# Kernel tuning notes

Measured on AMD Instinct MI355X. Metric: run time of the kernel, lower is better.

The kernel has to match this reference:

```python
import jax, jax.numpy as jnp
import numpy as np


def qz(x, width=8, frac=4):
    """Fixed-point fake-quant (MASE integer quantizer) with straight-through estimator."""
    step = 2.0 ** (-frac)
    lo = float(-(2 ** (width - 1)))
    hi = float(2 ** (width - 1) - 1)
    q = jnp.clip(jnp.round(x / step), lo, hi) * step
    return x + jax.lax.stop_gradient(q - x)


def qlinear(x, w, b=None):
    # quantize activations (8,4) and weights (8,7), dequantized GEMM
    y = qz(x, 8, 4) @ qz(w, 8, 7).T
    if b is not None:
        y = y + qz(b, 8, 7)
    return y


def setup_inputs() -> dict:
    key = jax.random.key(0)
    ks = jax.random.split(key, 14)
    B, N, C, HID = 4, 1024, 1024, 4096
    g = lambda k, shape, sc: jax.random.normal(k, shape, jnp.float32) * sc
    return {
        "x": g(ks[0], (B, N, C), 1.0),
        "q_w": g(ks[1], (C, C), 0.05),
        "kv_w": g(ks[2], (2 * C, C), 0.05),
        "proj_w": g(ks[3], (C, C), 0.05),
        "proj_b": jnp.zeros((C,), jnp.float32),
        "fc1_w": g(ks[4], (HID, C), 0.05),
        "fc1_b": jnp.zeros((HID,), jnp.float32),
        "fc2_w": g(ks[5], (C, HID), 0.05),
        "fc2_b": jnp.zeros((C,), jnp.float32),
        "aff1_w": g(ks[6], (1,), 1.0),
        "aff1_b": g(ks[7], (1,), 0.5),
        "aff2_w": g(ks[8], (1,), 1.0),
        "aff2_b": g(ks[9], (1,), 0.5),
    }


def reference(x, q_w, kv_w, proj_w, proj_b, fc1_w, fc1_b, fc2_w, fc2_b,
              aff1_w, aff1_b, aff2_w, aff2_b):
    B, N, C = x.shape
    H = 16
    D = C // H
    scale = D ** (-0.5)

    def affine(t, w, b):
        # quantized mul then quantized add (fixed_affine)
        t = qz(t, 8, 4) * qz(w, 8, 4)
        return qz(t, 8, 4) + qz(b, 8, 4)

    # ---- attention branch ----
    h = affine(x, aff1_w, aff1_b)
    q = qlinear(h, q_w).reshape(B, N, H, D).transpose(0, 2, 1, 3)      # [B,H,N,D]
    kv = qlinear(h, kv_w).reshape(B, N, 2, H, D).transpose(2, 0, 3, 1, 4)
    k, v = kv[0], kv[1]                                                 # [B,H,N,D]
    attn = jnp.einsum('bhnd,bhmd->bhnm', qz(q, 8, 4), qz(k, 8, 4))     # quant matmul
    attn = jax.nn.softmax(qz(attn * scale, 8, 4), axis=-1)             # QHashSoftmax
    attn = qz(attn, 8, 7)
    z = jnp.einsum('bhnm,bhmd->bhnd', qz(attn, 8, 7), qz(v, 8, 4))     # quant matmul
    z = z.transpose(0, 2, 1, 3).reshape(B, N, C)
    z = qlinear(z, proj_w, proj_b)
    x = qz(x, 8, 4) + qz(z, 8, 4)                                      # add1

    # ---- mlp branch ----
    h = affine(x, aff2_w, aff2_b)
    m = qlinear(h, fc1_w, fc1_b)
    m = qz(jax.nn.relu(m), 8, 4)                                       # quant relu
    m = qlinear(m, fc2_w, fc2_b)
    return qz(x, 8, 4) + qz(m, 8, 4)                                   # add2
```

## Files before the change

### kernel.cpp

```cpp
#include <hip/hip_runtime.h>

typedef unsigned short u16;
typedef __attribute__((ext_vector_type(4))) float f32x4;
typedef __attribute__((ext_vector_type(8))) short short8;
typedef __attribute__((ext_vector_type(4))) unsigned short u16x4;
typedef __attribute__((ext_vector_type(8))) unsigned short u16x8;

__device__ __forceinline__ float clampf(float x, float lo, float hi){ return fminf(fmaxf(x, lo), hi); }
__device__ __forceinline__ float qz44i(float x){ return clampf(rintf(x*16.f), -128.f, 127.f); }
__device__ __forceinline__ float qz44v(float x){ return qz44i(x)*0.0625f; }
__device__ __forceinline__ float qz87v(float x){ return clampf(rintf(x*128.f), -128.f, 127.f)*0.0078125f; }
__device__ __forceinline__ u16 bfbits(float f){ return (u16)(__float_as_uint(f) >> 16); }

__device__ __forceinline__ void gll16(const void* g, void* l){
  __builtin_amdgcn_global_load_lds((const __attribute__((address_space(1))) void*)g,
                                   (__attribute__((address_space(3))) void*)l, 16, 0, 0);
}

__global__ __launch_bounds__(256) void kquantw5(const float* __restrict__ w0, u16* __restrict__ o0,
                                                const float* __restrict__ w1, u16* __restrict__ o1,
                                                const float* __restrict__ w2, u16* __restrict__ o2,
                                                const float* __restrict__ w3, u16* __restrict__ o3,
                                                const float* __restrict__ w4, u16* __restrict__ o4){
  int v = blockIdx.x*256 + threadIdx.x;
  const float* w; u16* o; int base;
  if      (v <  262144){ w = w0; o = o0; base = 0;       }
  else if (v <  786432){ w = w1; o = o1; base = 262144;  }
  else if (v < 1048576){ w = w2; o = o2; base = 786432;  }
  else if (v < 2097152){ w = w3; o = o3; base = 1048576; }
  else                 { w = w4; o = o4; base = 2097152; }
  int i = (v - base)*4;
  float4 val = *(const float4*)(w + i);
  u16x4 r;
  r.x = bfbits(qz87v(val.x)); r.y = bfbits(qz87v(val.y));
  r.z = bfbits(qz87v(val.z)); r.w = bfbits(qz87v(val.w));
  *(u16x4*)(o + i) = r;
}

__global__ __launch_bounds__(256) void kaffine(const float* __restrict__ x, const float* __restrict__ aw,
                                               const float* __restrict__ ab, u16* __restrict__ o, int n){
  int i = (blockIdx.x*256 + threadIdx.x)*4;
  if (i >= n) return;
  float awv = qz44v(aw[0]);
  float abi = qz44i(ab[0]);
  float4 v = *(const float4*)(x + i);
  float in[4] = {v.x, v.y, v.z, v.w};
  u16x4 r;
  #pragma unroll
  for (int k=0;k<4;++k){
    float t  = qz44v(in[k]) * awv;
    float hi = clampf(qz44i(t) + abi, -128.f, 127.f);
    ((u16*)&r)[k] = bfbits(hi*0.0625f);
  }
  *(u16x4*)(o + i) = r;
}

__global__ __launch_bounds__(256) void ktransv(const u16* __restrict__ KVb, u16* __restrict__ VT){
  __shared__ u16 t[64][72];
  int nt = blockIdx.x;
  int bh = blockIdx.y;
  int b = bh >> 4, h = bh & 15;
  int tid = threadIdx.x;
  int nl = tid >> 2, d0 = (tid & 3)*16;
  const u16* src = KVb + (size_t)(b*1024 + nt*64 + nl)*2048 + 1024 + h*64 + d0;
  u16x8 v0 = *(const u16x8*)(src);
  u16x8 v1 = *(const u16x8*)(src + 8);
  #pragma unroll
  for (int k=0;k<8;++k) t[nl][d0+k]   = ((u16*)&v0)[k];
  #pragma unroll
  for (int k=0;k<8;++k) t[nl][d0+8+k] = ((u16*)&v1)[k];
  __syncthreads();
  int dl = tid >> 2, n0 = (tid & 3)*16;
  u16x8 o0, o1;
  #pragma unroll
  for (int k=0;k<8;++k) ((u16*)&o0)[k] = t[n0+k][dl];
  #pragma unroll
  for (int k=0;k<8;++k) ((u16*)&o1)[k] = t[n0+8+k][dl];
  u16* dst = VT + (size_t)bh*65536 + (size_t)dl*1024 + nt*64 + n0;
  *(u16x8*)(dst)     = o0;
  *(u16x8*)(dst + 8) = o1;
}

template<int EPI>
__global__ __launch_bounds__(256) void kgemm(
    const u16* __restrict__ A, const u16* __restrict__ Bw,
    const float* __restrict__ bias, const float* __restrict__ extra,
    u16* __restrict__ outB, float* __restrict__ outF,
    int M, int N, int K)
{
  __shared__ char As[128*64*2];
  __shared__ char Bs[128*64*2];
  const int tid = threadIdx.x, lane = tid & 63, w = tid >> 6;
  const int bm = blockIdx.y*128, bn = blockIdx.x*128;
  const int wr = (w>>1)*64, wc = (w&1)*64;
  const int srow = lane>>3;
  const int scol = (((lane&7) ^ srow) & 7)*8;
  const int mrow = lane & 15, kg = lane >> 4, swz = (lane & 7) << 4;

  const u16* Ab = A  + (size_t)bm*K;
  const u16* Bb = Bw + (size_t)bn*K;

  f32x4 acc[4][4];
  #pragma unroll
  for (int i=0;i<4;++i)
    #pragma unroll
    for (int j=0;j<4;++j) acc[i][j] = (f32x4){0.f,0.f,0.f,0.f};

  for (int k0 = 0; k0 < K; k0 += 64){
    #pragma unroll
    for (int c=0;c<4;++c){
      int ch = w*4 + c;
      int row = ch*8 + srow;
      gll16(Ab + (size_t)row*K + k0 + scol, As + ch*1024);
      gll16(Bb + (size_t)row*K + k0 + scol, Bs + ch*1024);
    }
    __syncthreads();
    #pragma unroll
    for (int ks=0; ks<2; ++ks){
      const int cb = (64*ks + 16*kg) ^ swz;
      short8 av[4], bv[4];
      #pragma unroll
      for (int i=0;i<4;++i) av[i] = *(const short8*)(As + (wr + i*16 + mrow)*128 + cb);
      #pragma unroll
      for (int j=0;j<4;++j) bv[j] = *(const short8*)(Bs + (wc + j*16 + mrow)*128 + cb);
      #pragma unroll
      for (int i=0;i<4;++i)
        #pragma unroll
        for (int j=0;j<4;++j)
          acc[i][j] = __builtin_amdgcn_mfma_f32_16x16x32_bf16(av[i], bv[j], acc[i][j], 0, 0, 0);
    }
    __syncthreads();
  }

  #pragma unroll
  for (int i=0;i<4;++i){
    #pragma unroll
    for (int j=0;j<4;++j){
      #pragma unroll
      for (int r=0;r<4;++r){
        int row = bm + wr + i*16 + 4*kg + r;
        int col = bn + wc + j*16 + mrow;
        float y = acc[i][j][r];
        size_t idx = (size_t)row*N + col;
        if (EPI == 0){
          outB[idx] = bfbits(qz44v(y));
        } else if (EPI == 1){
          y += qz87v(bias[col]);
          outF[idx] = qz44v(extra[idx]) + qz44v(y);
        } else if (EPI == 2){
          y += qz87v(bias[col]);
          y = fmaxf(y, 0.f);
          outB[idx] = bfbits(qz44v(y));
        } else {
          y += qz87v(bias[col]);
          outF[idx] = qz44v(extra[idx]) + qz44v(y);
        }
      }
    }
  }
}

__device__ __forceinline__ void compute_s(const char* Qs, const char* Ks,
                                          int w, int mrow, int kg, int swz, f32x4 (&s)[2][8]){
  short8 a[2][2];
  #pragma unroll
  for (int i=0;i<2;++i)
    #pragma unroll
    for (int ks=0;ks<2;++ks)
      a[i][ks] = *(const short8*)(Qs + (w*32 + i*16 + mrow)*128 + ((64*ks + 16*kg) ^ swz));
  #pragma unroll
  for (int i=0;i<2;++i)
    #pragma unroll
    for (int jf=0;jf<8;++jf) s[i][jf] = (f32x4){0.f,0.f,0.f,0.f};
  #pragma unroll
  for (int jf=0;jf<8;++jf){
    short8 b0 = *(const short8*)(Ks + (jf*16 + mrow)*128 + ((16*kg) ^ swz));
    short8 b1 = *(const short8*)(Ks + (jf*16 + mrow)*128 + ((64 + 16*kg) ^ swz));
    #pragma unroll
    for (int i=0;i<2;++i){
      s[i][jf] = __builtin_amdgcn_mfma_f32_16x16x32_bf16(a[i][0], b0, s[i][jf], 0, 0, 0);
      s[i][jf] = __builtin_amdgcn_mfma_f32_16x16x32_bf16(a[i][1], b1, s[i][jf], 0, 0, 0);
    }
  }
}

__global__ __launch_bounds__(256) void kattn(const u16* __restrict__ Qb, const u16* __restrict__ KVb,
                                             const u16* __restrict__ VT, u16* __restrict__ zq)
{
  __shared__ char Qs[128*128];
  __shared__ char Ks[128*128];
  __shared__ char Ps[128*256];
  __shared__ char Vs[64*256];
  const int tid = threadIdx.x, lane = tid & 63, w = tid >> 6;
  const int qt = blockIdx.x, bh = blockIdx.y;
  const int b = bh >> 4, h = bh & 15;
  const int srow = lane >> 3;
  const int scol = (((lane&7) ^ srow) & 7)*8;
  const int mrow = lane & 15, kg = lane >> 4, swz = (lane & 7) << 4;
  const size_t q0 = (size_t)(b*1024 + qt*128);

  #pragma unroll
  for (int c=0;c<4;++c){
    int ch = w*4 + c; int r = ch*8 + srow;
    gll16(Qb + (q0 + r)*1024 + h*64 + scol, Qs + ch*1024);
  }

  float m[2][4], Z[2][4];
  #pragma unroll
  for (int i=0;i<2;++i)
    #pragma unroll
    for (int r=0;r<4;++r){ m[i][r] = -3.0e38f; Z[i][r] = 0.f; }

  for (int kt=0; kt<8; ++kt){
    #pragma unroll
    for (int c=0;c<4;++c){
      int ch = w*4 + c; int r = ch*8 + srow;
      gll16(KVb + (size_t)(b*1024 + kt*128 + r)*2048 + h*64 + scol, Ks + ch*1024);
    }
    __syncthreads();
    f32x4 s[2][8];
    compute_s(Qs, Ks, w, mrow, kg, swz, s);
    #pragma unroll
    for (int i=0;i<2;++i){
      #pragma unroll
      for (int r=0;r<4;++r){
        float lv[8];
        float tmax = -3.0e38f;
        #pragma unroll
        for (int jf=0;jf<8;++jf){
          lv[jf] = clampf(rintf(s[i][jf][r]*2.f), -128.f, 127.f)*0.0625f;
          tmax = fmaxf(tmax, lv[jf]);
        }
        #pragma unroll
        for (int off=1; off<16; off<<=1) tmax = fmaxf(tmax, __shfl_xor(tmax, off));
        float ts = 0.f;
        #pragma unroll
        for (int jf=0;jf<8;++jf) ts += expf(lv[jf] - tmax);
        #pragma unroll
        for (int off=1; off<16; off<<=1) ts += __shfl_xor(ts, off);
        float mo = m[i][r];
        float mn = fmaxf(mo, tmax);
        Z[i][r] = Z[i][r]*expf(mo - mn) + ts*expf(tmax - mn);
        m[i][r] = mn;
      }
    }
    __syncthreads();
  }

  f32x4 zacc[2][4];
  #pragma unroll
  for (int i=0;i<2;++i)
    #pragma unroll
    for (int d=0;d<4;++d) zacc[i][d] = (f32x4){0.f,0.f,0.f,0.f};

  for (int kt=0; kt<8; ++kt){
    #pragma unroll
    for (int c=0;c<4;++c){
      int ch = w*4 + c; int r = ch*8 + srow;
      gll16(KVb + (size_t)(b*1024 + kt*128 + r)*2048 + h*64 + scol, Ks + ch*1024);
    }
    #pragma unroll
    for (int c=0;c<4;++c){
      int ch = w*4 + c; int dr = ch*4 + kg;
      int vx = ((lane&15) ^ (dr & 7))*8;
      gll16(VT + (size_t)bh*65536 + (size_t)dr*1024 + kt*128 + vx, Vs + ch*1024);
    }
    __syncthreads();
    f32x4 s[2][8];
    compute_s(Qs, Ks, w, mrow, kg, swz, s);
    #pragma unroll
    for (int i=0;i<2;++i){
      #pragma unroll
      for (int r=0;r<4;++r){
        float mm = m[i][r], zz = Z[i][r];
        int prow = w*32 + i*16 + 4*kg + r;
        int sw2 = (prow & 7) << 4;
        #pragma unroll
        for (int jf=0;jf<8;++jf){
          float lv = clampf(rintf(s[i][jf][r]*2.f), -128.f, 127.f)*0.0625f;
          float p = expf(lv - mm) / zz;
          float pi = fminf(rintf(p*128.f), 127.f);
          *(u16*)(Ps + prow*256 + (((jf*16 + mrow)*2) ^ sw2)) = bfbits(pi*0.0078125f);
        }
      }
    }
    __syncthreads();
    #pragma unroll
    for (int ms=0; ms<4; ++ms){
      const int cb = (64*ms + 16*kg) ^ swz;
      short8 pa0 = *(const short8*)(Ps + (w*32 +  0 + mrow)*256 + cb);
      short8 pa1 = *(const short8*)(Ps + (w*32 + 16 + mrow)*256 + cb);
      #pragma unroll
      for (int df=0; df<4; ++df){
        short8 vb = *(const short8*)(Vs + (df*16 + mrow)*256 + cb);
        zacc[0][df] = __builtin_amdgcn_mfma_f32_16x16x32_bf16(pa0, vb, zacc[0][df], 0, 0, 0);
        zacc[1][df] = __builtin_amdgcn_mfma_f32_16x16x32_bf16(pa1, vb, zacc[1][df], 0, 0, 0);
      }
    }
    __syncthreads();
  }

  #pragma unroll
  for (int i=0;i<2;++i){
    #pragma unroll
    for (int df=0; df<4; ++df){
      #pragma unroll
      for (int r=0;r<4;++r){
        int row = qt*128 + w*32 + i*16 + 4*kg + r;
        int col = df*16 + mrow;
        zq[((size_t)b*1024 + row)*1024 + h*64 + col] = bfbits(qz44v(zacc[i][df][r]));
      }
    }
  }
}

extern "C" void kernel_launch(void* const* d_in, const int* in_sizes, int n_in,
                              void* d_out, int out_size, void* d_ws, size_t ws_size,
                              hipStream_t stream) {
  const float* x      = (const float*)d_in[0];
  const float* q_w    = (const float*)d_in[1];
  const float* kv_w   = (const float*)d_in[2];
  const float* proj_w = (const float*)d_in[3];
  const float* proj_b = (const float*)d_in[4];
  const float* fc1_w  = (const float*)d_in[5];
  const float* fc1_b  = (const float*)d_in[6];
  const float* fc2_w  = (const float*)d_in[7];
  const float* fc2_b  = (const float*)d_in[8];
  const float* aff1_w = (const float*)d_in[9];
  const float* aff1_b = (const float*)d_in[10];
  const float* aff2_w = (const float*)d_in[11];
  const float* aff2_b = (const float*)d_in[12];

  char* ws = (char*)d_ws;
  const size_t MB = 1u << 20;
  u16*   wq_q  = (u16*)(ws + 0*MB);
  u16*   wq_kv = (u16*)(ws + 2*MB);
  u16*   wq_pj = (u16*)(ws + 6*MB);
  u16*   wq_f1 = (u16*)(ws + 8*MB);
  u16*   wq_f2 = (u16*)(ws + 16*MB);
  float* x1    = (float*)(ws + 24*MB);
  u16*   h1q   = (u16*)(ws + 40*MB);
  u16*   Qbuf  = (u16*)(ws + 48*MB);
  u16*   KVb   = (u16*)(ws + 56*MB);
  u16*   VT    = (u16*)(ws + 72*MB);
  u16*   mq    = (u16*)(ws + 56*MB);
  u16*   zq    = h1q;
  u16*   h2q   = Qbuf;

  kquantw5<<<12288, 256, 0, stream>>>(q_w, wq_q, kv_w, wq_kv, proj_w, wq_pj,
                                      fc1_w, wq_f1, fc2_w, wq_f2);

  kaffine<<<4096, 256, 0, stream>>>(x, aff1_w, aff1_b, h1q, 4096*1024);
  kgemm<0><<<dim3(8,32),  256, 0, stream>>>(h1q, wq_q,  nullptr, nullptr, Qbuf, nullptr, 4096, 1024, 1024);
  kgemm<0><<<dim3(16,32), 256, 0, stream>>>(h1q, wq_kv, nullptr, nullptr, KVb,  nullptr, 4096, 2048, 1024);
  ktransv<<<dim3(16,64), 256, 0, stream>>>(KVb, VT);
  kattn<<<dim3(8,64), 256, 0, stream>>>(Qbuf, KVb, VT, zq);
  kgemm<1><<<dim3(8,32),  256, 0, stream>>>(zq, wq_pj, proj_b, x, nullptr, x1, 4096, 1024, 1024);

  kaffine<<<4096, 256, 0, stream>>>(x1, aff2_w, aff2_b, h2q, 4096*1024);
  kgemm<2><<<dim3(32,32), 256, 0, stream>>>(h2q, wq_f1, fc1_b, nullptr, mq, nullptr, 4096, 4096, 1024);
  kgemm<3><<<dim3(8,32),  256, 0, stream>>>(mq, wq_f2, fc2_b, x1, nullptr, (float*)d_out, 4096, 1024, 4096);
}
```

Measured before the change: 456.2 us.

## Add 128x64 GEMM tile for N=1024 GEMMs and use exp lookup table in attention

Adds a kgemm64 kernel with a 128x64 output tile and uses it for the three N=1024 GEMMs (q, proj, fc2), doubling the grid to 512 blocks so more of the GPU's compute units are occupied. In attention, expf calls are replaced by a 256-entry shared-memory table indexed by integer logit differences, which works because the quantized logits fall on a 1/16 grid. V tiles are now read straight from global memory instead of being staged in LDS, and one barrier is removed. The direct V loads may be uncoalesced. The barrier between writing P and reading it appears to have no sync when a wave reads other waves' P rows, but each wave reads only its own rows, so it is probably safe. The exp_t table is written without a barrier before its first use, although the later barrier in the first loop covers it.

Result: faster. 427.0 us (-6.4%).

```diff
diff --git a/kernel.cpp b/kernel.cpp
--- a/kernel.cpp
+++ b/kernel.cpp
@@ -160,6 +160,90 @@
   }
 }
 
+template<int EPI>
+__global__ __launch_bounds__(256) void kgemm64(
+    const u16* __restrict__ A, const u16* __restrict__ Bw,
+    const float* __restrict__ bias, const float* __restrict__ extra,
+    u16* __restrict__ outB, float* __restrict__ outF,
+    int M, int N, int K)
+{
+  __shared__ char As[128*64*2];
+  __shared__ char Bs[64*64*2];
+  const int tid = threadIdx.x, lane = tid & 63, w = tid >> 6;
+  const int bm = blockIdx.y*128, bn = blockIdx.x*64;
+  const int wr = w*32;
+  const int srow = lane>>3;
+  const int scol = (((lane&7) ^ srow) & 7)*8;
+  const int mrow = lane & 15, kg = lane >> 4, swz = (lane & 7) << 4;
+
+  const u16* Ab = A  + (size_t)bm*K;
+  const u16* Bb = Bw + (size_t)bn*K;
+
+  f32x4 acc[2][4];
+  #pragma unroll
+  for (int i=0;i<2;++i)
+    #pragma unroll
+    for (int j=0;j<4;++j) acc[i][j] = (f32x4){0.f,0.f,0.f,0.f};
+
+  for (int k0 = 0; k0 < K; k0 += 64){
+    #pragma unroll
+    for (int c=0;c<4;++c){
+      int ch = w*4 + c;
+      int row = ch*8 + srow;
+      gll16(Ab + (size_t)row*K + k0 + scol, As + ch*1024);
+    }
+    #pragma unroll
+    for (int c=0;c<2;++c){
+      int ch = w*2 + c;
+      int row = ch*8 + srow;
+      gll16(Bb + (size_t)row*K + k0 + scol, Bs + ch*1024);
+    }
+    __syncthreads();
+    #pragma unroll
+    for (int ks=0; ks<2; ++ks){
+      const int cb = (64*ks + 16*kg) ^ swz;
+      short8 av[2], bv[4];
+      #pragma unroll
+      for (int i=0;i<2;++i) av[i] = *(const short8*)(As + (wr + i*16 + mrow)*128 + cb);
+      #pragma unroll
+      for (int j=0;j<4;++j) bv[j] = *(const short8*)(Bs + (j*16 + mrow)*128 + cb);
+      #pragma unroll
+      for (int i=0;i<2;++i)
+        #pragma unroll
+        for (int j=0;j<4;++j)
+          acc[i][j] = __builtin_amdgcn_mfma_f32_16x16x32_bf16(av[i], bv[j], acc[i][j], 0, 0, 0);
+    }
+    __syncthreads();
+  }
+
+  #pragma unroll
+  for (int i=0;i<2;++i){
+    #pragma unroll
+    for (int j=0;j<4;++j){
+      #pragma unroll
+      for (int r=0;r<4;++r){
+        int row = bm + wr + i*16 + 4*kg + r;
+        int col = bn + j*16 + mrow;
+        float y = acc[i][j][r];
+        size_t idx = (size_t)row*N + col;
+        if (EPI == 0){
+          outB[idx] = bfbits(qz44v(y));
+        } else if (EPI == 1){
+          y += qz87v(bias[col]);
+          outF[idx] = qz44v(extra[idx]) + qz44v(y);
+        } else if (EPI == 2){
+          y += qz87v(bias[col]);
+          y = fmaxf(y, 0.f);
+          outB[idx] = bfbits(qz44v(y));
+        } else {
+          y += qz87v(bias[col]);
+          outF[idx] = qz44v(extra[idx]) + qz44v(y);
+        }
+      }
+    }
+  }
+}
+
 __device__ __forceinline__ void compute_s(const char* Qs, const char* Ks,
                                           int w, int mrow, int kg, int swz, f32x4 (&s)[2][8]){
   short8 a[2][2];
@@ -190,7 +274,7 @@
   __shared__ char Qs[128*128];
   __shared__ char Ks[128*128];
   __shared__ char Ps[128*256];
-  __shared__ char Vs[64*256];
+  __shared__ float exp_t[256];
   const int tid = threadIdx.x, lane = tid & 63, w = tid >> 6;
   const int qt = blockIdx.x, bh = blockIdx.y;
   const int b = bh >> 4, h = bh & 15;
@@ -198,6 +282,9 @@
   const int scol = (((lane&7) ^ srow) & 7)*8;
   const int mrow = lane & 15, kg = lane >> 4, swz = (lane & 7) << 4;
   const size_t q0 = (size_t)(b*1024 + qt*128);
+  const u16* Vg = VT + (size_t)bh*65536;
+
+  exp_t[tid & 255] = expf(-(float)(tid & 255) * 0.0625f);
 
   #pragma unroll
   for (int c=0;c<4;++c){
@@ -209,7 +296,7 @@
   #pragma unroll
   for (int i=0;i<2;++i)
     #pragma unroll
-    for (int r=0;r<4;++r){ m[i][r] = -3.0e38f; Z[i][r] = 0.f; }
+    for (int r=0;r<4;++r){ m[i][r] = -128.f; Z[i][r] = 0.f; }
 
   for (int kt=0; kt<8; ++kt){
     #pragma unroll
@@ -224,23 +311,23 @@
     for (int i=0;i<2;++i){
       #pragma unroll
       for (int r=0;r<4;++r){
-        float lv[8];
-        float tmax = -3.0e38f;
+        float li[8];
+        float tm = -128.f;
         #pragma unroll
         for (int jf=0;jf<8;++jf){
-          lv[jf] = clampf(rintf(s[i][jf][r]*2.f), -128.f, 127.f)*0.0625f;
-          tmax = fmaxf(tmax, lv[jf]);
+          li[jf] = clampf(rintf(s[i][jf][r]*2.f), -128.f, 127.f);
+          tm = fmaxf(tm, li[jf]);
         }
         #pragma unroll
-        for (int off=1; off<16; off<<=1) tmax = fmaxf(tmax, __shfl_xor(tmax, off));
+        for (int off=1; off<16; off<<=1) tm = fmaxf(tm, __shfl_xor(tm, off));
         float ts = 0.f;
         #pragma unroll
-        for (int jf=0;jf<8;++jf) ts += expf(lv[jf] - tmax);
+        for (int jf=0;jf<8;++jf) ts += exp_t[(int)(tm - li[jf])];
         #pragma unroll
         for (int off=1; off<16; off<<=1) ts += __shfl_xor(ts, off);
         float mo = m[i][r];
-        float mn = fmaxf(mo, tmax);
-        Z[i][r] = Z[i][r]*expf(mo - mn) + ts*expf(tmax - mn);
+        float mn = fmaxf(mo, tm);
+        Z[i][r] = Z[i][r]*exp_t[(int)(mn - mo)] + ts*exp_t[(int)(mn - tm)];
         m[i][r] = mn;
       }
     }
@@ -259,12 +346,6 @@
       int ch = w*4 + c; int r = ch*8 + srow;
       gll16(KVb + (size_t)(b*1024 + kt*128 + r)*2048 + h*64 + scol, Ks + ch*1024);
     }
-    #pragma unroll
-    for (int c=0;c<4;++c){
-      int ch = w*4 + c; int dr = ch*4 + kg;
-      int vx = ((lane&15) ^ (dr & 7))*8;
-      gll16(VT + (size_t)bh*65536 + (size_t)dr*1024 + kt*128 + vx, Vs + ch*1024);
-    }
     __syncthreads();
     f32x4 s[2][8];
     compute_s(Qs, Ks, w, mrow, kg, swz, s);
@@ -272,19 +353,19 @@
     for (int i=0;i<2;++i){
       #pragma unroll
       for (int r=0;r<4;++r){
-        float mm = m[i][r], zz = Z[i][r];
+        float Mi = m[i][r], zz = Z[i][r];
         int prow = w*32 + i*16 + 4*kg + r;
         int sw2 = (prow & 7) << 4;
         #pragma unroll
         for (int jf=0;jf<8;++jf){
-          float lv = clampf(rintf(s[i][jf][r]*2.f), -128.f, 127.f)*0.0625f;
-          float p = expf(lv - mm) / zz;
+          float li = clampf(rintf(s[i][jf][r]*2.f), -128.f, 127.f);
+          float e = exp_t[(int)(Mi - li)];
+          float p = e / zz;
           float pi = fminf(rintf(p*128.f), 127.f);
           *(u16*)(Ps + prow*256 + (((jf*16 + mrow)*2) ^ sw2)) = bfbits(pi*0.0078125f);
         }
       }
     }
-    __syncthreads();
     #pragma unroll
     for (int ms=0; ms<4; ++ms){
       const int cb = (64*ms + 16*kg) ^ swz;
@@ -292,7 +373,7 @@
       short8 pa1 = *(const short8*)(Ps + (w*32 + 16 + mrow)*256 + cb);
       #pragma unroll
       for (int df=0; df<4; ++df){
-        short8 vb = *(const short8*)(Vs + (df*16 + mrow)*256 + cb);
+        short8 vb = *(const short8*)(Vg + (size_t)(df*16 + mrow)*1024 + kt*128 + 32*ms + 8*kg);
         zacc[0][df] = __builtin_amdgcn_mfma_f32_16x16x32_bf16(pa0, vb, zacc[0][df], 0, 0, 0);
         zacc[1][df] = __builtin_amdgcn_mfma_f32_16x16x32_bf16(pa1, vb, zacc[1][df], 0, 0, 0);
       }
@@ -351,13 +432,13 @@
                                       fc1_w, wq_f1, fc2_w, wq_f2);
 
   kaffine<<<4096, 256, 0, stream>>>(x, aff1_w, aff1_b, h1q, 4096*1024);
-  kgemm<0><<<dim3(8,32),  256, 0, stream>>>(h1q, wq_q,  nullptr, nullptr, Qbuf, nullptr, 4096, 1024, 1024);
-  kgemm<0><<<dim3(16,32), 256, 0, stream>>>(h1q, wq_kv, nullptr, nullptr, KVb,  nullptr, 4096, 2048, 1024);
+  kgemm64<0><<<dim3(16,32), 256, 0, stream>>>(h1q, wq_q,  nullptr, nullptr, Qbuf, nullptr, 4096, 1024, 1024);
+  kgemm<0><<<dim3(16,32),  256, 0, stream>>>(h1q, wq_kv, nullptr, nullptr, KVb,  nullptr, 4096, 2048, 1024);
   ktransv<<<dim3(16,64), 256, 0, stream>>>(KVb, VT);
   kattn<<<dim3(8,64), 256, 0, stream>>>(Qbuf, KVb, VT, zq);
-  kgemm<1><<<dim3(8,32),  256, 0, stream>>>(zq, wq_pj, proj_b, x, nullptr, x1, 4096, 1024, 1024);
+  kgemm64<1><<<dim3(16,32), 256, 0, stream>>>(zq, wq_pj, proj_b, x, nullptr, x1, 4096, 1024, 1024);
 
   kaffine<<<4096, 256, 0, stream>>>(x1, aff2_w, aff2_b, h2q, 4096*1024);
   kgemm<2><<<dim3(32,32), 256, 0, stream>>>(h2q, wq_f1, fc1_b, nullptr, mq, nullptr, 4096, 4096, 1024);
-  kgemm<3><<<dim3(8,32),  256, 0, stream>>>(mq, wq_f2, fc2_b, x1, nullptr, (float*)d_out, 4096, 1024, 4096);
-}
+  kgemm64<3><<<dim3(16,32), 256, 0, stream>>>(mq, wq_f2, fc2_b, x1, nullptr, (float*)d_out, 4096, 1024, 4096);
+}
```
